# Kernel tuning notes

Measured on AMD Instinct MI355X. Metric: run time of the kernel, lower is better.

Reference implementation:

```python
import jax, jax.numpy as jnp
import numpy as np

N_JOINTS = 21
N_DIMS = 3


def setup_inputs() -> dict:
    key = jax.random.key(0)
    k1, k2 = jax.random.split(key)
    B = 262144
    pred = jax.random.normal(k1, (B, N_JOINTS * N_DIMS), dtype=jnp.float32)
    target = jax.random.normal(k2, (B, N_JOINTS * N_DIMS), dtype=jnp.float32)
    return {"pred": pred, "target": target}


def reference(pred, target):
    # [B, 63] -> [B, 21, 3]; per-joint Euclidean distance, then mean over
    # joints and batch (mean-of-means over equal-sized groups == global mean).
    B = pred.shape[0]
    diff = pred.reshape(B, N_JOINTS, N_DIMS) - target.reshape(B, N_JOINTS, N_DIMS)
    dist = jnp.sqrt(jnp.sum(diff * diff, axis=-1))  # [B, 21]
    return jnp.mean(dist)
```

## Files before the change

kernel.cpp:

```cpp
#include <hip/hip_runtime.h>

#define NTHREADS 256
#define NBLOCKS 1792
#define TILE_F4 768
#define TILE_FLOATS 3072
#define TILE_TRIPLES 1024

__device__ __forceinline__ float wave_reduce(float v) {
    #pragma unroll
    for (int off = 32; off > 0; off >>= 1) v += __shfl_down(v, off, 64);
    return v;
}

__device__ __forceinline__ float block_reduce(float v) {
    v = wave_reduce(v);
    __shared__ float smem[NTHREADS / 64];
    const int lane = threadIdx.x & 63;
    const int wave = threadIdx.x >> 6;
    if (lane == 0) smem[wave] = v;
    __syncthreads();
    float s = 0.f;
    if (threadIdx.x == 0) {
        #pragma unroll
        for (int w = 0; w < NTHREADS / 64; ++w) s += smem[w];
    }
    return s;
}

__global__ __launch_bounds__(NTHREADS) void dis_partial_kernel(
    const float4* __restrict__ p4, const float4* __restrict__ t4,
    const float* __restrict__ pred, const float* __restrict__ targ,
    float* __restrict__ partials, int ntile, int ntrip) {
    __shared__ float diff[TILE_FLOATS];
    const int t = threadIdx.x;
    float acc = 0.f;

    for (int tile = blockIdx.x; tile < ntile; tile += gridDim.x) {
        const int base = tile * TILE_F4;
        #pragma unroll
        for (int j = 0; j < 3; ++j) {
            const int idx = base + j * NTHREADS + t;
            float4 p = p4[idx];
            float4 q = t4[idx];
            float4 d;
            d.x = p.x - q.x; d.y = p.y - q.y; d.z = p.z - q.z; d.w = p.w - q.w;
            ((float4*)diff)[j * NTHREADS + t] = d;
        }
        __syncthreads();
        #pragma unroll
        for (int j = 0; j < 4; ++j) {
            const int tr = j * NTHREADS + t;
            const float dx = diff[3 * tr + 0];
            const float dy = diff[3 * tr + 1];
            const float dz = diff[3 * tr + 2];
            acc += sqrtf(dx * dx + dy * dy + dz * dz);
        }
        __syncthreads();
    }

    for (int j = ntile * TILE_TRIPLES + blockIdx.x * NTHREADS + t; j < ntrip;
         j += gridDim.x * NTHREADS) {
        const float dx = pred[3 * j + 0] - targ[3 * j + 0];
        const float dy = pred[3 * j + 1] - targ[3 * j + 1];
        const float dz = pred[3 * j + 2] - targ[3 * j + 2];
        acc += sqrtf(dx * dx + dy * dy + dz * dz);
    }

    const float s = block_reduce(acc);
    if (threadIdx.x == 0) partials[blockIdx.x] = s;
}

__global__ __launch_bounds__(NTHREADS) void dis_finalize_kernel(
    const float* __restrict__ partials, float* __restrict__ out,
    int nblocks, float scale) {
    float acc = 0.f;
    for (int i = threadIdx.x; i < nblocks; i += NTHREADS) acc += partials[i];
    const float s = block_reduce(acc);
    if (threadIdx.x == 0) out[0] = s * scale;
}

extern "C" void kernel_launch(void* const* d_in, const int* in_sizes, int n_in,
                              void* d_out, int out_size, void* d_ws, size_t ws_size,
                              hipStream_t stream) {
    const float* pred = (const float*)d_in[0];
    const float* targ = (const float*)d_in[1];
    float* out = (float*)d_out;
    float* partials = (float*)d_ws;

    const int n = in_sizes[0];
    const int ntrip = n / 3;
    const int ntile = n / TILE_FLOATS;
    const float scale = 1.0f / (float)ntrip;

    dis_partial_kernel<<<NBLOCKS, NTHREADS, 0, stream>>>(
        (const float4*)pred, (const float4*)targ, pred, targ, partials, ntile, ntrip);
    dis_finalize_kernel<<<1, NTHREADS, 0, stream>>>(partials, out, NBLOCKS, scale);
}
```

Baseline: 143.2 us.

## Replace LDS-staged tiles with per-thread contiguous register loads of 8 triples

Drops the shared-memory transpose and barriers; each thread now loads six contiguous float4s from each input into registers and computes eight joint distances with two accumulators. The grid becomes one thread per chunk instead of a persistent fixed-block loop, which raises loads in flight. It trades per-instruction coalescing (96-byte thread stride) and a larger partials array for the finalize step.

```diff
diff --git a/kernel.cpp b/kernel.cpp
--- a/kernel.cpp
+++ b/kernel.cpp
@@ -1,10 +1,8 @@
 #include <hip/hip_runtime.h>
 
 #define NTHREADS 256
-#define NBLOCKS 1792
-#define TILE_F4 768
-#define TILE_FLOATS 3072
-#define TILE_TRIPLES 1024
+#define TRIP_PER_THREAD 8
+#define F4_PER_THREAD 6
 
 __device__ __forceinline__ float wave_reduce(float v) {
     #pragma unroll
@@ -27,46 +25,46 @@
     return s;
 }
 
-__global__ __launch_bounds__(NTHREADS) void dis_partial_kernel(
+__global__ __launch_bounds__(NTHREADS, 4) void dis_partial_kernel(
     const float4* __restrict__ p4, const float4* __restrict__ t4,
     const float* __restrict__ pred, const float* __restrict__ targ,
-    float* __restrict__ partials, int ntile, int ntrip) {
-    __shared__ float diff[TILE_FLOATS];
-    const int t = threadIdx.x;
-    float acc = 0.f;
+    float* __restrict__ partials, int nchunk, int ntrip) {
+    const int t = blockIdx.x * NTHREADS + threadIdx.x;
+    float acc0 = 0.f, acc1 = 0.f;
 
-    for (int tile = blockIdx.x; tile < ntile; tile += gridDim.x) {
-        const int base = tile * TILE_F4;
+    if (t < nchunk) {
+        alignas(16) float pv[24];
+        alignas(16) float tv[24];
+        const int base = F4_PER_THREAD * t;
         #pragma unroll
-        for (int j = 0; j < 3; ++j) {
-            const int idx = base + j * NTHREADS + t;
-            float4 p = p4[idx];
-            float4 q = t4[idx];
-            float4 d;
-            d.x = p.x - q.x; d.y = p.y - q.y; d.z = p.z - q.z; d.w = p.w - q.w;
-            ((float4*)diff)[j * NTHREADS + t] = d;
+        for (int j = 0; j < F4_PER_THREAD; ++j)
+            ((float4*)pv)[j] = p4[base + j];
+        #pragma unroll
+        for (int j = 0; j < F4_PER_THREAD; ++j)
+            ((float4*)tv)[j] = t4[base + j];
+
+        #pragma unroll
+        for (int k = 0; k < TRIP_PER_THREAD; k += 2) {
+            float dx0 = pv[3 * k + 0] - tv[3 * k + 0];
+            float dy0 = pv[3 * k + 1] - tv[3 * k + 1];
+            float dz0 = pv[3 * k + 2] - tv[3 * k + 2];
+            float dx1 = pv[3 * k + 3] - tv[3 * k + 3];
+            float dy1 = pv[3 * k + 4] - tv[3 * k + 4];
+            float dz1 = pv[3 * k + 5] - tv[3 * k + 5];
+            acc0 += sqrtf(dx0 * dx0 + dy0 * dy0 + dz0 * dz0);
+            acc1 += sqrtf(dx1 * dx1 + dy1 * dy1 + dz1 * dz1);
         }
-        __syncthreads();
-        #pragma unroll
-        for (int j = 0; j < 4; ++j) {
-            const int tr = j * NTHREADS + t;
-            const float dx = diff[3 * tr + 0];
-            const float dy = diff[3 * tr + 1];
-            const float dz = diff[3 * tr + 2];
-            acc += sqrtf(dx * dx + dy * dy + dz * dz);
-        }
-        __syncthreads();
     }
 
-    for (int j = ntile * TILE_TRIPLES + blockIdx.x * NTHREADS + t; j < ntrip;
+    for (int j = nchunk * TRIP_PER_THREAD + t; j < ntrip;
          j += gridDim.x * NTHREADS) {
         const float dx = pred[3 * j + 0] - targ[3 * j + 0];
         const float dy = pred[3 * j + 1] - targ[3 * j + 1];
         const float dz = pred[3 * j + 2] - targ[3 * j + 2];
-        acc += sqrtf(dx * dx + dy * dy + dz * dz);
+        acc0 += sqrtf(dx * dx + dy * dy + dz * dz);
     }
 
-    const float s = block_reduce(acc);
+    const float s = block_reduce(acc0 + acc1);
     if (threadIdx.x == 0) partials[blockIdx.x] = s;
 }
 
@@ -89,10 +87,12 @@
 
     const int n = in_sizes[0];
     const int ntrip = n / 3;
-    const int ntile = n / TILE_FLOATS;
+    const int nchunk = n / (3 * TRIP_PER_THREAD);
+    const int nblocks = (nchunk + NTHREADS - 1) / NTHREADS;
     const float scale = 1.0f / (float)ntrip;
 
-    dis_partial_kernel<<<NBLOCKS, NTHREADS, 0, stream>>>(
-        (const float4*)pred, (const float4*)targ, pred, targ, partials, ntile, ntrip);
-    dis_finalize_kernel<<<1, NTHREADS, 0, stream>>>(partials, out, NBLOCKS, scale);
+    dis_partial_kernel<<<nblocks, NTHREADS, 0, stream>>>(
+        (const float4*)pred, (const float4*)targ, pred, targ, partials,
+        nchunk, ntrip);
+    dis_finalize_kernel<<<1, NTHREADS, 0, stream>>>(partials, out, nblocks, scale);
 }
```

Measured after the change: 143.9 us. Within noise of the previous version (+0.5%).
